# Performance work log

Hardware: AMD Instinct MI355X
Metric: run time of the kernel (lower is better)

The kernel has to match this reference:

```python
import jax, jax.numpy as jnp
import numpy as np

B, S, D, H = 2, 2048, 1024, 16
HD = D // H

def setup_inputs() -> dict:
    key = jax.random.key(0)
    ks = jax.random.split(key, 5)
    scale = 1.0 / np.sqrt(D)
    x = jax.random.normal(ks[0], (B, S, D), dtype=jnp.float32)
    W_qkv = jax.random.normal(ks[1], (D, 3 * D), dtype=jnp.float32) * scale
    b_qkv = jnp.zeros((3 * D,), dtype=jnp.float32)
    W_proj = jax.random.normal(ks[2], (D, D), dtype=jnp.float32) * scale
    b_proj = jnp.zeros((D,), dtype=jnp.float32)
    return {"x": x, "W_qkv": W_qkv, "b_qkv": b_qkv, "W_proj": W_proj, "b_proj": b_proj}

def reference(x, W_qkv, b_qkv, W_proj, b_proj):
    # qkv projection: [B,S,3D]
    qkv = jnp.einsum('bsd,df->bsf', x, W_qkv) + b_qkv
    q, k, v = jnp.split(qkv, 3, axis=-1)
    # reshape to heads: [B,H,S,hd]
    q = q.reshape(B, S, H, HD).transpose(0, 2, 1, 3)
    k = k.reshape(B, S, H, HD).transpose(0, 2, 1, 3)
    v = v.reshape(B, S, H, HD).transpose(0, 2, 1, 3)
    scores = jnp.einsum('bhqd,bhkd->bhqk', q, k) / jnp.sqrt(jnp.float32(HD))
    attn = jax.nn.softmax(scores, axis=-1)
    out = jnp.einsum('bhqk,bhkd->bhqd', attn, v)
    out = out.transpose(0, 2, 1, 3).reshape(B, S, D)
    return jnp.einsum('bsd,df->bsf', out, W_proj) + b_proj
```

## Files before the change

### kernel.cpp

```cpp
#include <hip/hip_runtime.h>

#define BATCH 2
#define SLEN 2048
#define DMODEL 1024
#define NHEAD 16
#define HDIM 64
#define MROWS (BATCH * SLEN)

typedef __attribute__((ext_vector_type(8))) short bf16x8;
typedef __attribute__((ext_vector_type(4))) short bf16x4;
typedef __attribute__((ext_vector_type(4))) float f32x4;
typedef __attribute__((ext_vector_type(8))) _Float16 f16x8;
typedef __attribute__((ext_vector_type(4))) _Float16 f16x4;

__device__ inline short f2bf(float x) {
    union { float f; unsigned u; } v; v.f = x;
    unsigned r = (v.u + 0x7FFFu + ((v.u >> 16) & 1u)) >> 16;
    return (short)r;
}
__device__ inline float bf2f(short h) {
    union { unsigned u; float f; } v; v.u = ((unsigned)(unsigned short)h) << 16;
    return v.f;
}
__device__ inline unsigned fbits(float x) {
    union { float f; unsigned u; } v; v.f = x; return v.u;
}
__device__ inline float hw_exp2(float x) {
    float r;
    asm("v_exp_f32 %0, %1" : "=v"(r) : "v"(x));
    return r;
}

__global__ __launch_bounds__(256) void cast_f16(
    const float* __restrict__ in, _Float16* __restrict__ out, int n4)
{
    int i = blockIdx.x * 256 + threadIdx.x;
    if (i >= n4) return;
    float4 f = ((const float4*)in)[i];
    f16x4 h;
    h[0] = (_Float16)f.x; h[1] = (_Float16)f.y;
    h[2] = (_Float16)f.z; h[3] = (_Float16)f.w;
    ((f16x4*)out)[i] = h;
}

__global__ __launch_bounds__(256) void transpose_f16(
    const float* __restrict__ in, _Float16* __restrict__ outT, int K, int N)
{
    __shared__ float T[64][68];
    const int tid = threadIdx.x;
    const int n0 = blockIdx.x * 64, k0 = blockIdx.y * 64;
#pragma unroll
    for (int i = 0; i < 4; i++) {
        int idx = tid + i * 256;
        int r = idx >> 4, c4 = idx & 15;
        *(float4*)&T[r][c4 * 4] = *(const float4*)&in[(size_t)(k0 + r) * N + n0 + c4 * 4];
    }
    __syncthreads();
#pragma unroll
    for (int i = 0; i < 4; i++) {
        int idx = tid + i * 256;
        int n = idx >> 4, kg = idx & 15;
        f16x4 h;
#pragma unroll
        for (int j = 0; j < 4; j++)
            h[j] = (_Float16)T[kg * 4 + j][n];
        *(f16x4*)&outT[(size_t)(n0 + n) * K + k0 + kg * 4] = h;
    }
}

__global__ __launch_bounds__(256) void transpose_v(
    const short* __restrict__ qkv, short* __restrict__ vT)
{
    __shared__ short T[64 * 68];
    const int tid = threadIdx.x;
    const int bid = blockIdx.x;
    const int st = bid & 31, h = (bid >> 5) & 15, b = bid >> 9;
    const int s0 = st * 64;
    const short* src = qkv + (size_t)b * SLEN * (3 * DMODEL) + 2 * DMODEL + h * HDIM;

    const int srow = tid >> 3, sc8 = tid & 7;
#pragma unroll
    for (int it = 0; it < 2; it++) {
        int s = srow + it * 32;
        *(bf16x8*)&T[s * 68 + sc8 * 8] =
            *(const bf16x8*)&src[(size_t)(s0 + s) * (3 * DMODEL) + sc8 * 8];
    }
    __syncthreads();

    const int d = tid >> 2, sq = tid & 3;
    short* dst = vT + ((size_t)(b * NHEAD + h) * HDIM + d) * SLEN + s0 + sq * 16;
    bf16x8 o0, o1;
#pragma unroll
    for (int j = 0; j < 8; j++) {
        o0[j] = T[(sq * 16 + j) * 68 + d];
        o1[j] = T[(sq * 16 + 8 + j) * 68 + d];
    }
    *(bf16x8*)&dst[0] = o0;
    *(bf16x8*)&dst[8] = o1;
}

#define GSTR 40

template<int OUT_BF16>
__global__ __launch_bounds__(256) void gemm_f16(
    const _Float16* __restrict__ A, const _Float16* __restrict__ Bw,
    const float* __restrict__ bias, void* __restrict__ Cout,
    int M, int N, int K)
{
    __shared__ _Float16 As[128 * GSTR], Bs[128 * GSTR];

    const int tid  = threadIdx.x;
    const int wave = tid >> 6, lane = tid & 63;
    const int quad = lane >> 4, lr = lane & 15;
    const int wm = (wave >> 1) * 64, wn = (wave & 1) * 64;
    const int row0 = blockIdx.y * 128, col0 = blockIdx.x * 128;

    f32x4 acc[4][4];
#pragma unroll
    for (int i = 0; i < 4; i++)
#pragma unroll
        for (int j = 0; j < 4; j++) acc[i][j] = (f32x4){0.f, 0.f, 0.f, 0.f};

    const int sr = tid >> 2, sc = tid & 3;

    const _Float16* ap0 = A  + (size_t)(row0 + sr) * K + sc * 8;
    const _Float16* ap1 = ap0 + (size_t)64 * K;
    const _Float16* bp0 = Bw + (size_t)(col0 + sr) * K + sc * 8;
    const _Float16* bp1 = bp0 + (size_t)64 * K;

    f16x8 apre[2], bpre[2];
    apre[0] = *(const f16x8*)ap0; apre[1] = *(const f16x8*)ap1;
    bpre[0] = *(const f16x8*)bp0; bpre[1] = *(const f16x8*)bp1;
    ap0 += 32; ap1 += 32; bp0 += 32; bp1 += 32;

    const int ls = sr * GSTR + sc * 8;

    for (int k0 = 0; k0 < K; k0 += 32) {
        *(f16x8*)&As[ls] = apre[0];
        *(f16x8*)&As[ls + 64 * GSTR] = apre[1];
        *(f16x8*)&Bs[ls] = bpre[0];
        *(f16x8*)&Bs[ls + 64 * GSTR] = bpre[1];

        if (k0 + 32 < K) {
            apre[0] = *(const f16x8*)ap0; apre[1] = *(const f16x8*)ap1;
            bpre[0] = *(const f16x8*)bp0; bpre[1] = *(const f16x8*)bp1;
            ap0 += 32; ap1 += 32; bp0 += 32; bp1 += 32;
        }

        __syncthreads();

        f16x8 af[4];
#pragma unroll
        for (int mt = 0; mt < 4; mt++)
            af[mt] = *(const f16x8*)&As[(wm + mt * 16 + lr) * GSTR + quad * 8];
#pragma unroll
        for (int nt = 0; nt < 4; nt++) {
            f16x8 b = *(const f16x8*)&Bs[(wn + nt * 16 + lr) * GSTR + quad * 8];
#pragma unroll
            for (int mt = 0; mt < 4; mt++)
                acc[mt][nt] = __builtin_amdgcn_mfma_f32_16x16x32_f16(af[mt], b, acc[mt][nt], 0, 0, 0);
        }

        __syncthreads();
    }

#pragma unroll
    for (int mt = 0; mt < 4; mt++) {
#pragma unroll
        for (int nt = 0; nt < 4; nt++) {
            int col = col0 + wn + nt * 16 + lr;
            float bv = bias[col];
#pragma unroll
            for (int r = 0; r < 4; r++) {
                int row = row0 + wm + mt * 16 + quad * 4 + r;
                float v = acc[mt][nt][r] + bv;
                if (OUT_BF16)
                    ((short*)Cout)[(size_t)row * N + col] = f2bf(v);
                else
                    ((float*)Cout)[(size_t)row * N + col] = v;
            }
        }
    }
}

#define ASTR 72
#define NT   (SLEN / 64)
#define RSTR 20
#define QK_SCALE_LOG2E 0.1803368801111244f

__global__ __launch_bounds__(256) void attn_mfma(
    const short* __restrict__ qkv, const short* __restrict__ vT,
    _Float16* __restrict__ attn)
{
    __shared__ __align__(16) char smem[2 * 64 * ASTR * 2 * 2];
    short* KsBuf = (short*)smem;
    short* VtBuf = KsBuf + 2 * 64 * ASTR;

    const int tid  = threadIdx.x;
    const int lane = tid & 63;
    const int wave = tid >> 6;
    const int quad = lane >> 4;
    const int lr   = lane & 15;
    const int qhalf  = wave >> 1;
    const int cthalf = wave & 1;

    const int bid = blockIdx.x;
    const int qt = bid & 31;
    const int h  = (bid >> 5) & 15;
    const int b  = bid >> 9;
    const int q0 = qt * 64;

    const short* qbase = qkv + (size_t)b * SLEN * (3 * DMODEL) + h * HDIM;
    const short* kbase = qbase + DMODEL;
    const short* vtbase = vT + (size_t)(b * NHEAD + h) * HDIM * SLEN;

    bf16x8 qf[2][2];
#pragma unroll
    for (int qs = 0; qs < 2; qs++)
#pragma unroll
        for (int ds2 = 0; ds2 < 2; ds2++) {
            bf16x8 q = *(const bf16x8*)&qbase[(size_t)(q0 + qhalf * 32 + qs * 16 + lr) * (3 * DMODEL) + ds2 * 32 + quad * 8];
#pragma unroll
            for (int j = 0; j < 8; j++)
                q[j] = f2bf(bf2f(q[j]) * QK_SCALE_LOG2E);
            qf[qs][ds2] = q;
        }

    bf16x4 ones;
#pragma unroll
    for (int j = 0; j < 4; j++) ones[j] = (short)0x3F80;

    f32x4 oacc[2][4];
#pragma unroll
    for (int qs = 0; qs < 2; qs++)
#pragma unroll
        for (int t = 0; t < 4; t++) oacc[qs][t] = (f32x4){0.f, 0.f, 0.f, 0.f};
    f32x4 sacc[2] = {{0.f, 0.f, 0.f, 0.f}, {0.f, 0.f, 0.f, 0.f}};

    const int srow = tid >> 3, sc8 = tid & 7;

    const short* kp0 = kbase + (size_t)srow * (3 * DMODEL) + sc8 * 8;
    const short* kp1 = kp0 + 32 * (3 * DMODEL);
    const short* vp0 = vtbase + (size_t)srow * SLEN + sc8 * 8;
    const short* vp1 = vp0 + 32 * SLEN;

    bf16x8 kpre[2], vpre[2];
    kpre[0] = *(const bf16x8*)kp0; kpre[1] = *(const bf16x8*)kp1;
    vpre[0] = *(const bf16x8*)vp0; vpre[1] = *(const bf16x8*)vp1;
    kp0 += 64 * (3 * DMODEL); kp1 += 64 * (3 * DMODEL);
    vp0 += 64; vp1 += 64;

    for (int kt = 0; kt < NT; kt++) {
        const int cur = kt & 1;
        short* ks = KsBuf + cur * 64 * ASTR;
        short* vt = VtBuf + cur * 64 * ASTR;

        *(bf16x8*)&ks[srow * ASTR + sc8 * 8] = kpre[0];
        *(bf16x8*)&ks[(srow + 32) * ASTR + sc8 * 8] = kpre[1];
        *(bf16x8*)&vt[srow * ASTR + sc8 * 8] = vpre[0];
        *(bf16x8*)&vt[(srow + 32) * ASTR + sc8 * 8] = vpre[1];

        if (kt + 1 < NT) {
            kpre[0] = *(const bf16x8*)kp0; kpre[1] = *(const bf16x8*)kp1;
            vpre[0] = *(const bf16x8*)vp0; vpre[1] = *(const bf16x8*)vp1;
            kp0 += 64 * (3 * DMODEL); kp1 += 64 * (3 * DMODEL);
            vp0 += 64; vp1 += 64;
        }

        __syncthreads();

#pragma unroll
        for (int ct2 = 0; ct2 < 2; ct2++) {
            const int ct = cthalf * 2 + ct2;
            bf16x8 kf0 = *(const bf16x8*)&ks[(ct * 16 + lr) * ASTR + quad * 8];
            bf16x8 kf1 = *(const bf16x8*)&ks[(ct * 16 + lr) * ASTR + 32 + quad * 8];
            bf16x4 vf0 = *(const bf16x4*)&vt[(0 * 16 + lr) * ASTR + ct * 16 + quad * 4];
            bf16x4 vf1 = *(const bf16x4*)&vt[(1 * 16 + lr) * ASTR + ct * 16 + quad * 4];
            bf16x4 vf2 = *(const bf16x4*)&vt[(2 * 16 + lr) * ASTR + ct * 16 + quad * 4];
            bf16x4 vf3 = *(const bf16x4*)&vt[(3 * 16 + lr) * ASTR + ct * 16 + quad * 4];

#pragma unroll
            for (int qs = 0; qs < 2; qs++) {
                f32x4 st = {0.f, 0.f, 0.f, 0.f};
                st = __builtin_amdgcn_mfma_f32_16x16x32_bf16(kf0, qf[qs][0], st, 0, 0, 0);
                st = __builtin_amdgcn_mfma_f32_16x16x32_bf16(kf1, qf[qs][1], st, 0, 0, 0);

                float p0[4];
#pragma unroll
                for (int r = 0; r < 4; r++) p0[r] = hw_exp2(st[r]);
                union { uint2 u; bf16x4 v; } pk0;
                pk0.u.x = __builtin_amdgcn_perm(fbits(p0[1]), fbits(p0[0]), 0x07060302u);
                pk0.u.y = __builtin_amdgcn_perm(fbits(p0[3]), fbits(p0[2]), 0x07060302u);
                bf16x4 pf0 = pk0.v;

                sacc[qs] = __builtin_amdgcn_mfma_f32_16x16x16bf16_1k(ones, pf0, sacc[qs], 0, 0, 0);
                oacc[qs][0] = __builtin_amdgcn_mfma_f32_16x16x16bf16_1k(vf0, pf0, oacc[qs][0], 0, 0, 0);
                oacc[qs][1] = __builtin_amdgcn_mfma_f32_16x16x16bf16_1k(vf1, pf0, oacc[qs][1], 0, 0, 0);
                oacc[qs][2] = __builtin_amdgcn_mfma_f32_16x16x16bf16_1k(vf2, pf0, oacc[qs][2], 0, 0, 0);
                oacc[qs][3] = __builtin_amdgcn_mfma_f32_16x16x16bf16_1k(vf3, pf0, oacc[qs][3], 0, 0, 0);
            }
        }
    }

    __syncthreads();
    float* Lf = (float*)smem;
    float* myrow = Lf + (wave * 64 + lane) * RSTR;

    if (cthalf == 1) {
        *(f32x4*)&myrow[0]  = oacc[0][0];
        *(f32x4*)&myrow[4]  = oacc[0][1];
        *(f32x4*)&myrow[8]  = oacc[0][2];
        *(f32x4*)&myrow[12] = oacc[0][3];
        myrow[16] = sacc[0][0];
    }
    __syncthreads();
    if (cthalf == 0) {
        const float* pr = Lf + ((wave ^ 1) * 64 + lane) * RSTR;
        f32x4 o0 = oacc[0][0] + *(const f32x4*)&pr[0];
        f32x4 o1 = oacc[0][1] + *(const f32x4*)&pr[4];
        f32x4 o2 = oacc[0][2] + *(const f32x4*)&pr[8];
        f32x4 o3 = oacc[0][3] + *(const f32x4*)&pr[12];
        const float inv = 1.0f / (sacc[0][0] + pr[16]);
        const int row = b * SLEN + q0 + qhalf * 32 + lr;
        f16x4 h4;
#pragma unroll
        for (int r = 0; r < 4; r++) h4[r] = (_Float16)(o0[r] * inv);
        *(f16x4*)&attn[(size_t)row * DMODEL + h * HDIM + 0 * 16 + quad * 4] = h4;
#pragma unroll
        for (int r = 0; r < 4; r++) h4[r] = (_Float16)(o1[r] * inv);
        *(f16x4*)&attn[(size_t)row * DMODEL + h * HDIM + 1 * 16 + quad * 4] = h4;
#pragma unroll
        for (int r = 0; r < 4; r++) h4[r] = (_Float16)(o2[r] * inv);
        *(f16x4*)&attn[(size_t)row * DMODEL + h * HDIM + 2 * 16 + quad * 4] = h4;
#pragma unroll
        for (int r = 0; r < 4; r++) h4[r] = (_Float16)(o3[r] * inv);
        *(f16x4*)&attn[(size_t)row * DMODEL + h * HDIM + 3 * 16 + quad * 4] = h4;
        *(f32x4*)&myrow[0]  = oacc[1][0];
        *(f32x4*)&myrow[4]  = oacc[1][1];
        *(f32x4*)&myrow[8]  = oacc[1][2];
        *(f32x4*)&myrow[12] = oacc[1][3];
        myrow[16] = sacc[1][0];
    }
    __syncthreads();
    if (cthalf == 1) {
        const float* pr = Lf + ((wave ^ 1) * 64 + lane) * RSTR;
        f32x4 o0 = oacc[1][0] + *(const f32x4*)&pr[0];
        f32x4 o1 = oacc[1][1] + *(const f32x4*)&pr[4];
        f32x4 o2 = oacc[1][2] + *(const f32x4*)&pr[8];
        f32x4 o3 = oacc[1][3] + *(const f32x4*)&pr[12];
        const float inv = 1.0f / (sacc[1][0] + pr[16]);
        const int row = b * SLEN + q0 + qhalf * 32 + 16 + lr;
        f16x4 h4;
#pragma unroll
        for (int r = 0; r < 4; r++) h4[r] = (_Float16)(o0[r] * inv);
        *(f16x4*)&attn[(size_t)row * DMODEL + h * HDIM + 0 * 16 + quad * 4] = h4;
#pragma unroll
        for (int r = 0; r < 4; r++) h4[r] = (_Float16)(o1[r] * inv);
        *(f16x4*)&attn[(size_t)row * DMODEL + h * HDIM + 1 * 16 + quad * 4] = h4;
#pragma unroll
        for (int r = 0; r < 4; r++) h4[r] = (_Float16)(o2[r] * inv);
        *(f16x4*)&attn[(size_t)row * DMODEL + h * HDIM + 2 * 16 + quad * 4] = h4;
#pragma unroll
        for (int r = 0; r < 4; r++) h4[r] = (_Float16)(o3[r] * inv);
        *(f16x4*)&attn[(size_t)row * DMODEL + h * HDIM + 3 * 16 + quad * 4] = h4;
    }
}

extern "C" void kernel_launch(void* const* d_in, const int* in_sizes, int n_in,
                              void* d_out, int out_size, void* d_ws, size_t ws_size,
                              hipStream_t stream) {
    (void)in_sizes; (void)n_in; (void)out_size; (void)ws_size;
    const float* x     = (const float*)d_in[0];
    const float* Wqkv  = (const float*)d_in[1];
    const float* bqkv  = (const float*)d_in[2];
    const float* Wproj = (const float*)d_in[3];
    const float* bproj = (const float*)d_in[4];
    float* out = (float*)d_out;

    short* qkv = (short*)d_ws;
    _Float16* xf = (_Float16*)(qkv + (size_t)MROWS * 3 * DMODEL);
    _Float16* wq = xf + (size_t)MROWS * DMODEL;
    _Float16* wp = wq + (size_t)3 * DMODEL * DMODEL;
    short* vT = (short*)(wp + (size_t)DMODEL * DMODEL);
    _Float16* attnb = (_Float16*)(vT + (size_t)MROWS * DMODEL);

    cast_f16<<<dim3(MROWS * DMODEL / 4 / 256), 256, 0, stream>>>(x, xf, MROWS * DMODEL / 4);
    transpose_f16<<<dim3(3 * DMODEL / 64, DMODEL / 64), 256, 0, stream>>>(Wqkv, wq, DMODEL, 3 * DMODEL);
    transpose_f16<<<dim3(DMODEL / 64, DMODEL / 64), 256, 0, stream>>>(Wproj, wp, DMODEL, DMODEL);

    gemm_f16<1><<<dim3(3 * DMODEL / 128, MROWS / 128), 256, 0, stream>>>(
        xf, wq, bqkv, (void*)qkv, MROWS, 3 * DMODEL, DMODEL);

    transpose_v<<<dim3(BATCH * NHEAD * (SLEN / 64)), 256, 0, stream>>>(qkv, vT);

    attn_mfma<<<dim3(BATCH * NHEAD * (SLEN / 64)), 256, 0, stream>>>(qkv, vT, attnb);

    gemm_f16<0><<<dim3(DMODEL / 128, MROWS / 128), 256, 0, stream>>>(
        attnb, wp, bproj, (void*)out, MROWS, DMODEL, DMODEL);
}
```

Before: 206.2 us.

## Merge cast/transpose prep kernels into one launch and deepen GEMM K-tile

The fp16 cast of x and the two weight transposes now run in a single kernel that dispatches on block index, removing two kernel launches and their inter-launch gaps. The GEMM K tile grows from 32 to 64 per iteration with a padded LDS stride of 72, halving the number of barrier pairs and global prefetch rounds. In exchange it uses more LDS and registers per block, which may lower occupancy.

```diff
diff --git a/kernel.cpp b/kernel.cpp
--- a/kernel.cpp
+++ b/kernel.cpp
@@ -31,24 +31,41 @@
     return r;
 }
 
-__global__ __launch_bounds__(256) void cast_f16(
-    const float* __restrict__ in, _Float16* __restrict__ out, int n4)
-{
-    int i = blockIdx.x * 256 + threadIdx.x;
-    if (i >= n4) return;
-    float4 f = ((const float4*)in)[i];
-    f16x4 h;
-    h[0] = (_Float16)f.x; h[1] = (_Float16)f.y;
-    h[2] = (_Float16)f.z; h[3] = (_Float16)f.w;
-    ((f16x4*)out)[i] = h;
-}
-
-__global__ __launch_bounds__(256) void transpose_f16(
-    const float* __restrict__ in, _Float16* __restrict__ outT, int K, int N)
+#define NCAST (MROWS * DMODEL / 4 / 256)
+#define NTW1  ((3 * DMODEL / 64) * (DMODEL / 64))
+#define NTW2  ((DMODEL / 64) * (DMODEL / 64))
+
+__global__ __launch_bounds__(256) void prep(
+    const float* __restrict__ x, _Float16* __restrict__ xf,
+    const float* __restrict__ Wqkv, _Float16* __restrict__ wq,
+    const float* __restrict__ Wproj, _Float16* __restrict__ wp)
 {
     __shared__ float T[64][68];
+    int bid = blockIdx.x;
     const int tid = threadIdx.x;
-    const int n0 = blockIdx.x * 64, k0 = blockIdx.y * 64;
+
+    if (bid < NCAST) {
+        int i = bid * 256 + tid;
+        float4 f = ((const float4*)x)[i];
+        f16x4 h;
+        h[0] = (_Float16)f.x; h[1] = (_Float16)f.y;
+        h[2] = (_Float16)f.z; h[3] = (_Float16)f.w;
+        ((f16x4*)xf)[i] = h;
+        return;
+    }
+    bid -= NCAST;
+
+    const float* in; _Float16* outT; int N; int n0, k0;
+    if (bid < NTW1) {
+        in = Wqkv; outT = wq; N = 3 * DMODEL;
+        n0 = (bid % 48) * 64; k0 = (bid / 48) * 64;
+    } else {
+        bid -= NTW1;
+        in = Wproj; outT = wp; N = DMODEL;
+        n0 = (bid % 16) * 64; k0 = (bid / 16) * 64;
+    }
+    const int K = DMODEL;
+
 #pragma unroll
     for (int i = 0; i < 4; i++) {
         int idx = tid + i * 256;
@@ -99,7 +116,7 @@
     *(bf16x8*)&dst[8] = o1;
 }
 
-#define GSTR 40
+#define GSTR2 72
 
 template<int OUT_BF16>
 __global__ __launch_bounds__(256) void gemm_f16(
@@ -107,7 +124,7 @@
     const float* __restrict__ bias, void* __restrict__ Cout,
     int M, int N, int K)
 {
-    __shared__ _Float16 As[128 * GSTR], Bs[128 * GSTR];
+    __shared__ _Float16 As[128 * GSTR2], Bs[128 * GSTR2];
 
     const int tid  = threadIdx.x;
     const int wave = tid >> 6, lane = tid & 63;
@@ -128,37 +145,48 @@
     const _Float16* bp0 = Bw + (size_t)(col0 + sr) * K + sc * 8;
     const _Float16* bp1 = bp0 + (size_t)64 * K;
 
-    f16x8 apre[2], bpre[2];
-    apre[0] = *(const f16x8*)ap0; apre[1] = *(const f16x8*)ap1;
-    bpre[0] = *(const f16x8*)bp0; bpre[1] = *(const f16x8*)bp1;
-    ap0 += 32; ap1 += 32; bp0 += 32; bp1 += 32;
-
-    const int ls = sr * GSTR + sc * 8;
-
-    for (int k0 = 0; k0 < K; k0 += 32) {
-        *(f16x8*)&As[ls] = apre[0];
-        *(f16x8*)&As[ls + 64 * GSTR] = apre[1];
-        *(f16x8*)&Bs[ls] = bpre[0];
-        *(f16x8*)&Bs[ls + 64 * GSTR] = bpre[1];
-
-        if (k0 + 32 < K) {
-            apre[0] = *(const f16x8*)ap0; apre[1] = *(const f16x8*)ap1;
-            bpre[0] = *(const f16x8*)bp0; bpre[1] = *(const f16x8*)bp1;
-            ap0 += 32; ap1 += 32; bp0 += 32; bp1 += 32;
+    f16x8 apre[4], bpre[4];
+    apre[0] = *(const f16x8*)ap0;        apre[1] = *(const f16x8*)(ap0 + 32);
+    apre[2] = *(const f16x8*)ap1;        apre[3] = *(const f16x8*)(ap1 + 32);
+    bpre[0] = *(const f16x8*)bp0;        bpre[1] = *(const f16x8*)(bp0 + 32);
+    bpre[2] = *(const f16x8*)bp1;        bpre[3] = *(const f16x8*)(bp1 + 32);
+    ap0 += 64; ap1 += 64; bp0 += 64; bp1 += 64;
+
+    const int ls = sr * GSTR2 + sc * 8;
+
+    for (int k0 = 0; k0 < K; k0 += 64) {
+        *(f16x8*)&As[ls]                    = apre[0];
+        *(f16x8*)&As[ls + 32]               = apre[1];
+        *(f16x8*)&As[ls + 64 * GSTR2]       = apre[2];
+        *(f16x8*)&As[ls + 64 * GSTR2 + 32]  = apre[3];
+        *(f16x8*)&Bs[ls]                    = bpre[0];
+        *(f16x8*)&Bs[ls + 32]               = bpre[1];
+        *(f16x8*)&Bs[ls + 64 * GSTR2]       = bpre[2];
+        *(f16x8*)&Bs[ls + 64 * GSTR2 + 32]  = bpre[3];
+
+        if (k0 + 64 < K) {
+            apre[0] = *(const f16x8*)ap0;        apre[1] = *(const f16x8*)(ap0 + 32);
+            apre[2] = *(const f16x8*)ap1;        apre[3] = *(const f16x8*)(ap1 + 32);
+            bpre[0] = *(const f16x8*)bp0;        bpre[1] = *(const f16x8*)(bp0 + 32);
+            bpre[2] = *(const f16x8*)bp1;        bpre[3] = *(const f16x8*)(bp1 + 32);
+            ap0 += 64; ap1 += 64; bp0 += 64; bp1 += 64;
         }
 
         __syncthreads();
 
-        f16x8 af[4];
-#pragma unroll
-        for (int mt = 0; mt < 4; mt++)
-            af[mt] = *(const f16x8*)&As[(wm + mt * 16 + lr) * GSTR + quad * 8];
-#pragma unroll
-        for (int nt = 0; nt < 4; nt++) {
-            f16x8 b = *(const f16x8*)&Bs[(wn + nt * 16 + lr) * GSTR + quad * 8];
+#pragma unroll
+        for (int kk = 0; kk < 2; kk++) {
+            f16x8 af[4];
 #pragma unroll
             for (int mt = 0; mt < 4; mt++)
-                acc[mt][nt] = __builtin_amdgcn_mfma_f32_16x16x32_f16(af[mt], b, acc[mt][nt], 0, 0, 0);
+                af[mt] = *(const f16x8*)&As[(wm + mt * 16 + lr) * GSTR2 + kk * 32 + quad * 8];
+#pragma unroll
+            for (int nt = 0; nt < 4; nt++) {
+                f16x8 b = *(const f16x8*)&Bs[(wn + nt * 16 + lr) * GSTR2 + kk * 32 + quad * 8];
+#pragma unroll
+                for (int mt = 0; mt < 4; mt++)
+                    acc[mt][nt] = __builtin_amdgcn_mfma_f32_16x16x32_f16(af[mt], b, acc[mt][nt], 0, 0, 0);
+            }
         }
 
         __syncthreads();
@@ -384,9 +412,7 @@
     short* vT = (short*)(wp + (size_t)DMODEL * DMODEL);
     _Float16* attnb = (_Float16*)(vT + (size_t)MROWS * DMODEL);
 
-    cast_f16<<<dim3(MROWS * DMODEL / 4 / 256), 256, 0, stream>>>(x, xf, MROWS * DMODEL / 4);
-    transpose_f16<<<dim3(3 * DMODEL / 64, DMODEL / 64), 256, 0, stream>>>(Wqkv, wq, DMODEL, 3 * DMODEL);
-    transpose_f16<<<dim3(DMODEL / 64, DMODEL / 64), 256, 0, stream>>>(Wproj, wp, DMODEL, DMODEL);
+    prep<<<dim3(NCAST + NTW1 + NTW2), 256, 0, stream>>>(x, xf, Wqkv, wq, Wproj, wp);
 
     gemm_f16<1><<<dim3(3 * DMODEL / 128, MROWS / 128), 256, 0, stream>>>(
         xf, wq, bqkv, (void*)qkv, MROWS, 3 * DMODEL, DMODEL);
```

Result: faster. 196.3 us (-4.8%).
